# Optimization experiments

Measured on AMD Instinct MI355X. Metric: run time of the kernel, lower is better.

Reference implementation:

```python
import jax, jax.numpy as jnp
import numpy as np

B, S, H, R = 2, 1024, 512, 64


def setup_inputs() -> dict:
    key = jax.random.key(0)
    k1, k2, k3 = jax.random.split(key, 3)
    hidden_states = jax.random.normal(k1, (B, S, H), dtype=jnp.float32)
    # all_indices is the row-major cartesian product (seq_idx, hidden_idx),
    # as required by the final .view(batch, seq_len, hidden_size) in the module.
    si = jnp.repeat(jnp.arange(S, dtype=jnp.int64), H)
    hi = jnp.tile(jnp.arange(H, dtype=jnp.int64), S)
    all_indices = jnp.stack([si, hi], axis=1)  # [S*H, 2]
    W_seq = jax.random.normal(k2, (R, H), dtype=jnp.float32) * (1.0 / np.sqrt(H))
    hidden_embeddings = jax.random.normal(k3, (H, R), dtype=jnp.float32) * 0.02
    cp_weight = jnp.ones((1, R), dtype=jnp.float32)  # CP buffer, all ones
    return {
        "hidden_states": hidden_states,
        "all_indices": all_indices,
        "W_seq": W_seq,
        "hidden_embeddings": hidden_embeddings,
        "cp_weight": cp_weight,
    }


def reference(hidden_states, all_indices, W_seq, hidden_embeddings, cp_weight):
    b, s, h = hidden_states.shape
    # seq_mode_factor: Linear(hidden_size -> rank), no bias
    seq_emb = jnp.einsum("bsh,rh->bsr", hidden_states, W_seq)  # [B,S,R]
    si = all_indices[:, 0]  # [N]
    hi = all_indices[:, 1]  # [N]
    # Fold the (all-ones) CP weight into the hidden-mode factor, then
    # gather + hadamard + rank reduction in one fused expression.
    hid_fac = hidden_embeddings * cp_weight[0][None, :]  # [H,R]
    out = jnp.einsum("bnr,nr->bn", seq_emb[:, si, :], hid_fac[hi, :])  # [B,N]
    n = all_indices.shape[0]
    return out.reshape(b, s, n // s)  # [B,S,H], out_units=1 squeezed
```

## Files before the change

kernel.cpp:

```cpp
#include <hip/hip_runtime.h>


#define Hd 512
#define Rd 64
#define ROWS 8
#define THREADS 256

__global__ __launch_bounds__(THREADS) void cp_fused(
    const float* __restrict__ hs,
    const float* __restrict__ W,
    const float* __restrict__ he,
    const float* __restrict__ cp,
    float* __restrict__ out)
{
    __shared__ float s_hs[ROWS][Hd];
    __shared__ float s_E[ROWS][Rd];
    __shared__ float s_cp[Rd];

    const int t = threadIdx.x;
    const size_t row0 = (size_t)blockIdx.x * ROWS;

    const float4* hs4 = (const float4*)(hs + row0 * Hd);
    float4* s_hs4 = (float4*)&s_hs[0][0];
#pragma unroll
    for (int i = 0; i < 4; ++i)
        s_hs4[t + i * THREADS] = hs4[t + i * THREADS];
    if (t < Rd) s_cp[t] = cp[t];
    __syncthreads();

    {
        const int r = t >> 2;
        const int q = t & 3;
        float acc[ROWS];
#pragma unroll
        for (int i = 0; i < ROWS; ++i) acc[i] = 0.f;
        const float4* w4 = (const float4*)(W + r * Hd + q * 128);
#pragma unroll 8
        for (int j = 0; j < 32; ++j) {
            const float4 w = w4[j];
#pragma unroll
            for (int i = 0; i < ROWS; ++i) {
                const float4 x = ((const float4*)&s_hs[i][q * 128])[j];
                acc[i] += w.x * x.x + w.y * x.y + w.z * x.z + w.w * x.w;
            }
        }
#pragma unroll
        for (int i = 0; i < ROWS; ++i) {
            acc[i] += __shfl_xor(acc[i], 1);
            acc[i] += __shfl_xor(acc[i], 2);
        }
        if (q == 0) {
#pragma unroll
            for (int i = 0; i < ROWS; ++i) s_E[i][r] = acc[i];
        }
    }
    __syncthreads();

#pragma unroll
    for (int hh = 0; hh < 2; ++hh) {
        const int h = t + hh * THREADS;
        float o[ROWS];
#pragma unroll
        for (int i = 0; i < ROWS; ++i) o[i] = 0.f;
        const float4* he4 = (const float4*)(he + h * Rd);
#pragma unroll
        for (int j = 0; j < 16; ++j) {
            float4 f = he4[j];
            f.x *= s_cp[4 * j + 0];
            f.y *= s_cp[4 * j + 1];
            f.z *= s_cp[4 * j + 2];
            f.w *= s_cp[4 * j + 3];
#pragma unroll
            for (int i = 0; i < ROWS; ++i) {
                o[i] += s_E[i][4 * j + 0] * f.x + s_E[i][4 * j + 1] * f.y
                      + s_E[i][4 * j + 2] * f.z + s_E[i][4 * j + 3] * f.w;
            }
        }
#pragma unroll
        for (int i = 0; i < ROWS; ++i)
            out[(row0 + i) * Hd + h] = o[i];
    }
}

extern "C" void kernel_launch(void* const* d_in, const int* in_sizes, int n_in,
                              void* d_out, int out_size, void* d_ws, size_t ws_size,
                              hipStream_t stream) {
    const float* hs = (const float*)d_in[0];
    const float* W  = (const float*)d_in[2];
    const float* he = (const float*)d_in[3];
    const float* cp = (const float*)d_in[4];
    float* out = (float*)d_out;

    const int n_rows = 2 * 1024;
    cp_fused<<<dim3(n_rows / ROWS), dim3(THREADS), 0, stream>>>(hs, W, he, cp, out);
}
```

Baseline: 87.88 us.

## Stage W and hidden embeddings through padded shared memory with register prefetch

Both matmul phases now stream their weight matrices (W_seq, then hidden_embeddings) through a padded shared-memory buffer in four chunks. The next chunk is prefetched into registers while the current one is computed. Work is remapped so each thread reads one padded weight row from LDS against a broadcast activation row: two sequence rows per wave in phase one, four output rows per thread in phase two. This removes the strided per-thread global loads and the cross-lane shuffle reduction, at the cost of extra syncs and about 34KB more shared memory, which could reduce occupancy.

```diff
diff --git a/kernel.cpp b/kernel.cpp
--- a/kernel.cpp
+++ b/kernel.cpp
@@ -4,9 +4,11 @@
 #define Hd 512
 #define Rd 64
 #define ROWS 8
-#define THREADS 256
+#define T 256
+#define WPAD 132
+#define HPAD 68
 
-__global__ __launch_bounds__(THREADS) void cp_fused(
+__global__ __launch_bounds__(T) void cp_fused_v2(
     const float* __restrict__ hs,
     const float* __restrict__ W,
     const float* __restrict__ he,
@@ -14,71 +16,99 @@
     float* __restrict__ out)
 {
     __shared__ float s_hs[ROWS][Hd];
+    __shared__ float s_buf[128 * HPAD];
     __shared__ float s_E[ROWS][Rd];
     __shared__ float s_cp[Rd];
 
     const int t = threadIdx.x;
+    const int lane = t & 63;
+    const int w = t >> 6;
     const size_t row0 = (size_t)blockIdx.x * ROWS;
 
     const float4* hs4 = (const float4*)(hs + row0 * Hd);
     float4* s_hs4 = (float4*)&s_hs[0][0];
 #pragma unroll
-    for (int i = 0; i < 4; ++i)
-        s_hs4[t + i * THREADS] = hs4[t + i * THREADS];
+    for (int i = 0; i < 4; ++i) s_hs4[t + i * T] = hs4[t + i * T];
     if (t < Rd) s_cp[t] = cp[t];
-    __syncthreads();
 
-    {
-        const int r = t >> 2;
-        const int q = t & 3;
-        float acc[ROWS];
+    const int rw = t >> 5;
+    const int q4 = t & 31;
+
+    float4 pfw[8];
 #pragma unroll
-        for (int i = 0; i < ROWS; ++i) acc[i] = 0.f;
-        const float4* w4 = (const float4*)(W + r * Hd + q * 128);
-#pragma unroll 8
+    for (int k = 0; k < 8; ++k)
+        pfw[k] = ((const float4*)W)[(rw + 8 * k) * 128 + q4];
+
+    const int r0 = 2 * w, r1 = 2 * w + 1;
+    float acc0 = 0.f, acc1 = 0.f;
+
+    for (int c = 0; c < 4; ++c) {
+        __syncthreads();
+#pragma unroll
+        for (int k = 0; k < 8; ++k)
+            *(float4*)&s_buf[(rw + 8 * k) * WPAD + 4 * q4] = pfw[k];
+        __syncthreads();
+        if (c < 3) {
+#pragma unroll
+            for (int k = 0; k < 8; ++k)
+                pfw[k] = ((const float4*)W)[(rw + 8 * k) * 128 + (c + 1) * 32 + q4];
+        }
+        const float* wrow = &s_buf[lane * WPAD];
+        const float* h0p = &s_hs[r0][c * 128];
+        const float* h1p = &s_hs[r1][c * 128];
+#pragma unroll
         for (int j = 0; j < 32; ++j) {
-            const float4 w = w4[j];
-#pragma unroll
-            for (int i = 0; i < ROWS; ++i) {
-                const float4 x = ((const float4*)&s_hs[i][q * 128])[j];
-                acc[i] += w.x * x.x + w.y * x.y + w.z * x.z + w.w * x.w;
-            }
-        }
-#pragma unroll
-        for (int i = 0; i < ROWS; ++i) {
-            acc[i] += __shfl_xor(acc[i], 1);
-            acc[i] += __shfl_xor(acc[i], 2);
-        }
-        if (q == 0) {
-#pragma unroll
-            for (int i = 0; i < ROWS; ++i) s_E[i][r] = acc[i];
+            const float4 wt = *(const float4*)&wrow[4 * j];
+            const float4 a  = *(const float4*)&h0p[4 * j];
+            const float4 b  = *(const float4*)&h1p[4 * j];
+            acc0 += wt.x * a.x + wt.y * a.y + wt.z * a.z + wt.w * a.w;
+            acc1 += wt.x * b.x + wt.y * b.y + wt.z * b.z + wt.w * b.w;
         }
     }
-    __syncthreads();
+    const float cpl = s_cp[lane];
+    s_E[r0][lane] = acc0 * cpl;
+    s_E[r1][lane] = acc1 * cpl;
 
+    float4 pfh[8];
 #pragma unroll
-    for (int hh = 0; hh < 2; ++hh) {
-        const int h = t + hh * THREADS;
-        float o[ROWS];
+    for (int k = 0; k < 8; ++k)
+        pfh[k] = ((const float4*)he)[t + k * T];
+
+    const int hl = t & 127;
+    const int rb = (t >> 7) * 4;
+
+    for (int c = 0; c < 4; ++c) {
+        __syncthreads();
 #pragma unroll
-        for (int i = 0; i < ROWS; ++i) o[i] = 0.f;
-        const float4* he4 = (const float4*)(he + h * Rd);
+        for (int k = 0; k < 8; ++k) {
+            const int f = t + k * T;
+            *(float4*)&s_buf[(f >> 4) * HPAD + 4 * (f & 15)] = pfh[k];
+        }
+        __syncthreads();
+        if (c < 3) {
+#pragma unroll
+            for (int k = 0; k < 8; ++k)
+                pfh[k] = ((const float4*)he)[(c + 1) * 2048 + t + k * T];
+        }
+        float o0 = 0.f, o1 = 0.f, o2 = 0.f, o3 = 0.f;
+        const float* hrow = &s_buf[hl * HPAD];
 #pragma unroll
         for (int j = 0; j < 16; ++j) {
-            float4 f = he4[j];
-            f.x *= s_cp[4 * j + 0];
-            f.y *= s_cp[4 * j + 1];
-            f.z *= s_cp[4 * j + 2];
-            f.w *= s_cp[4 * j + 3];
-#pragma unroll
-            for (int i = 0; i < ROWS; ++i) {
-                o[i] += s_E[i][4 * j + 0] * f.x + s_E[i][4 * j + 1] * f.y
-                      + s_E[i][4 * j + 2] * f.z + s_E[i][4 * j + 3] * f.w;
-            }
+            const float4 hf = *(const float4*)&hrow[4 * j];
+            const float4 e0 = *(const float4*)&s_E[rb + 0][4 * j];
+            const float4 e1 = *(const float4*)&s_E[rb + 1][4 * j];
+            const float4 e2 = *(const float4*)&s_E[rb + 2][4 * j];
+            const float4 e3 = *(const float4*)&s_E[rb + 3][4 * j];
+            o0 += hf.x * e0.x + hf.y * e0.y + hf.z * e0.z + hf.w * e0.w;
+            o1 += hf.x * e1.x + hf.y * e1.y + hf.z * e1.z + hf.w * e1.w;
+            o2 += hf.x * e2.x + hf.y * e2.y + hf.z * e2.z + hf.w * e2.w;
+            o3 += hf.x * e3.x + hf.y * e3.y + hf.z * e3.z + hf.w * e3.w;
         }
-#pragma unroll
-        for (int i = 0; i < ROWS; ++i)
-            out[(row0 + i) * Hd + h] = o[i];
+        float* op = out + (row0 + rb) * Hd + c * 128 + hl;
+        op[0 * Hd] = o0;
+        op[1 * Hd] = o1;
+        op[2 * Hd] = o2;
+        op[3 * Hd] = o3;
     }
 }
 
@@ -91,6 +121,5 @@
     const float* cp = (const float*)d_in[4];
     float* out = (float*)d_out;
 
-    const int n_rows = 2 * 1024;
-    cp_fused<<<dim3(n_rows / ROWS), dim3(THREADS), 0, stream>>>(hs, W, he, cp, out);
+    cp_fused_v2<<<dim3(2048 / ROWS), dim3(T), 0, stream>>>(hs, W, he, cp, out);
 }
```

After: 92.75 us. +5.6%, slower.

## Precompute combined hidden-to-hidden matrix and replace low-rank path with single GEMM

Applied to the files above, without the earlier changes.

Splits the work into two kernels: one that folds W_seq, the CP weight and the hidden embeddings into a dense HxH matrix K in workspace, and a GEMM kernel that multiplies hidden_states by K with a split-K reduction through shared memory. This removes the two-stage rank-64 contraction and its intermediate synchronization. In exchange it raises arithmetic per row about fourfold, adds a second launch and writes and reads a 1 MB intermediate.

```diff
diff --git a/kernel.cpp b/kernel.cpp
--- a/kernel.cpp
+++ b/kernel.cpp
@@ -3,82 +3,114 @@
 
 #define Hd 512
 #define Rd 64
-#define ROWS 8
-#define THREADS 256
 
-__global__ __launch_bounds__(THREADS) void cp_fused(
-    const float* __restrict__ hs,
+__global__ __launch_bounds__(256) void cp_precompute_K(
     const float* __restrict__ W,
     const float* __restrict__ he,
     const float* __restrict__ cp,
+    float* __restrict__ K)
+{
+    __shared__ float s_W[8][Rd];
+    __shared__ float s_he[128 * 65];
+
+    const int t = threadIdx.x;
+    const int hp0 = blockIdx.x * 8;
+
+    {
+        const int i = t & 7, r = t >> 3;
+        s_W[i][r]      = W[r * Hd + hp0 + i] * cp[r];
+        s_W[i][r + 32] = W[(r + 32) * Hd + hp0 + i] * cp[r + 32];
+    }
+
+    const int hl = t & 127;
+    const int ig = (t >> 7) * 4;
+
+    for (int hc = 0; hc < 4; ++hc) {
+        __syncthreads();
+        const float4* src = (const float4*)(he + (size_t)hc * 128 * Rd);
+#pragma unroll
+        for (int k = 0; k < 8; ++k) {
+            const int f = t + k * 256;
+            const int h = f >> 4, r4 = f & 15;
+            const float4 v = src[f];
+            float* d = &s_he[h * 65 + 4 * r4];
+            d[0] = v.x; d[1] = v.y; d[2] = v.z; d[3] = v.w;
+        }
+        __syncthreads();
+
+        float a0 = 0.f, a1 = 0.f, a2 = 0.f, a3 = 0.f;
+        const float* hrow = &s_he[hl * 65];
+#pragma unroll
+        for (int r = 0; r < Rd; ++r) {
+            const float hv = hrow[r];
+            a0 += hv * s_W[ig + 0][r];
+            a1 += hv * s_W[ig + 1][r];
+            a2 += hv * s_W[ig + 2][r];
+            a3 += hv * s_W[ig + 3][r];
+        }
+        const int h = hc * 128 + hl;
+        K[(hp0 + ig + 0) * Hd + h] = a0;
+        K[(hp0 + ig + 1) * Hd + h] = a1;
+        K[(hp0 + ig + 2) * Hd + h] = a2;
+        K[(hp0 + ig + 3) * Hd + h] = a3;
+    }
+}
+
+__global__ __launch_bounds__(512) void cp_gemm(
+    const float* __restrict__ hs,
+    const float* __restrict__ K,
     float* __restrict__ out)
 {
-    __shared__ float s_hs[ROWS][Hd];
-    __shared__ float s_E[ROWS][Rd];
-    __shared__ float s_cp[Rd];
+    __shared__ float s_hs[8][Hd];
+    __shared__ float2 s_red[256][9];
 
     const int t = threadIdx.x;
-    const size_t row0 = (size_t)blockIdx.x * ROWS;
-
-    const float4* hs4 = (const float4*)(hs + row0 * Hd);
-    float4* s_hs4 = (float4*)&s_hs[0][0];
-#pragma unroll
-    for (int i = 0; i < 4; ++i)
-        s_hs4[t + i * THREADS] = hs4[t + i * THREADS];
-    if (t < Rd) s_cp[t] = cp[t];
-    __syncthreads();
+    const size_t row0 = (size_t)blockIdx.x * 8;
 
     {
-        const int r = t >> 2;
-        const int q = t & 3;
-        float acc[ROWS];
-#pragma unroll
-        for (int i = 0; i < ROWS; ++i) acc[i] = 0.f;
-        const float4* w4 = (const float4*)(W + r * Hd + q * 128);
-#pragma unroll 8
-        for (int j = 0; j < 32; ++j) {
-            const float4 w = w4[j];
-#pragma unroll
-            for (int i = 0; i < ROWS; ++i) {
-                const float4 x = ((const float4*)&s_hs[i][q * 128])[j];
-                acc[i] += w.x * x.x + w.y * x.y + w.z * x.z + w.w * x.w;
-            }
-        }
-#pragma unroll
-        for (int i = 0; i < ROWS; ++i) {
-            acc[i] += __shfl_xor(acc[i], 1);
-            acc[i] += __shfl_xor(acc[i], 2);
-        }
-        if (q == 0) {
-#pragma unroll
-            for (int i = 0; i < ROWS; ++i) s_E[i][r] = acc[i];
-        }
+        const float4* src = (const float4*)(hs + row0 * Hd);
+        float4* dst = (float4*)&s_hs[0][0];
+        dst[t] = src[t];
+        dst[t + 512] = src[t + 512];
     }
     __syncthreads();
 
+    const int hcol = t & 255;
+    const int half = t >> 8;
+    const int hpB = half * 256;
+
+    float2 acc[8];
 #pragma unroll
-    for (int hh = 0; hh < 2; ++hh) {
-        const int h = t + hh * THREADS;
-        float o[ROWS];
+    for (int i = 0; i < 8; ++i) acc[i] = make_float2(0.f, 0.f);
+
+    const float2* K2 = (const float2*)K;
+
+    for (int hp = 0; hp < 256; hp += 4) {
+        float2 kv0 = K2[(hpB + hp + 0) * 256 + hcol];
+        float2 kv1 = K2[(hpB + hp + 1) * 256 + hcol];
+        float2 kv2 = K2[(hpB + hp + 2) * 256 + hcol];
+        float2 kv3 = K2[(hpB + hp + 3) * 256 + hcol];
 #pragma unroll
-        for (int i = 0; i < ROWS; ++i) o[i] = 0.f;
-        const float4* he4 = (const float4*)(he + h * Rd);
+        for (int i = 0; i < 8; ++i) {
+            const float4 a = *(const float4*)&s_hs[i][hpB + hp];
+            acc[i].x += a.x * kv0.x + a.y * kv1.x + a.z * kv2.x + a.w * kv3.x;
+            acc[i].y += a.x * kv0.y + a.y * kv1.y + a.z * kv2.y + a.w * kv3.y;
+        }
+    }
+
+    if (half == 1) {
 #pragma unroll
-        for (int j = 0; j < 16; ++j) {
-            float4 f = he4[j];
-            f.x *= s_cp[4 * j + 0];
-            f.y *= s_cp[4 * j + 1];
-            f.z *= s_cp[4 * j + 2];
-            f.w *= s_cp[4 * j + 3];
+        for (int i = 0; i < 8; ++i) s_red[hcol][i] = acc[i];
+    }
+    __syncthreads();
+    if (half == 0) {
 #pragma unroll
-            for (int i = 0; i < ROWS; ++i) {
-                o[i] += s_E[i][4 * j + 0] * f.x + s_E[i][4 * j + 1] * f.y
-                      + s_E[i][4 * j + 2] * f.z + s_E[i][4 * j + 3] * f.w;
-            }
+        for (int i = 0; i < 8; ++i) {
+            const float2 p = s_red[hcol][i];
+            acc[i].x += p.x;
+            acc[i].y += p.y;
+            *(float2*)&out[(row0 + i) * Hd + 2 * hcol] = acc[i];
         }
-#pragma unroll
-        for (int i = 0; i < ROWS; ++i)
-            out[(row0 + i) * Hd + h] = o[i];
     }
 }
 
@@ -90,7 +122,8 @@
     const float* he = (const float*)d_in[3];
     const float* cp = (const float*)d_in[4];
     float* out = (float*)d_out;
+    float* Kbuf = (float*)d_ws;
 
-    const int n_rows = 2 * 1024;
-    cp_fused<<<dim3(n_rows / ROWS), dim3(THREADS), 0, stream>>>(hs, W, he, cp, out);
+    cp_precompute_K<<<dim3(64), dim3(256), 0, stream>>>(W, he, cp, Kbuf);
+    cp_gemm<<<dim3(256), dim3(512), 0, stream>>>(hs, Kbuf, out);
 }
```

Measured after the change: 115.5 us. 1.31x slower.

## Precompute combined weight matrix and run single bf16 MFMA GEMM

Applied to the files above, without the earlier changes.

Reassociates the two chained projections by first building K = (he*cp)·W as a 512x512 bf16 matrix in a small kernel, then computing out = hs·K^T with a bf16 MFMA GEMM. This removes the rank-64 intermediate and the per-block reload of W and he in favour of tensor-core matrix ops with a swizzled tile order. It adds a second launch and workspace traffic, raises FLOPs (512x512 inner product instead of two rank-64 passes), and lowers precision by rounding both hs and K to bf16.

```diff
diff --git a/kernel.cpp b/kernel.cpp
--- a/kernel.cpp
+++ b/kernel.cpp
@@ -1,85 +1,78 @@
 #include <hip/hip_runtime.h>
 
 
-#define Hd 512
-#define Rd 64
-#define ROWS 8
-#define THREADS 256
+typedef __bf16 bf16x8 __attribute__((ext_vector_type(8)));
+typedef float f32x4 __attribute__((ext_vector_type(4)));
 
-__global__ __launch_bounds__(THREADS) void cp_fused(
-    const float* __restrict__ hs,
+__global__ __launch_bounds__(256) void cp_K(
     const float* __restrict__ W,
     const float* __restrict__ he,
     const float* __restrict__ cp,
-    float* __restrict__ out)
+    __bf16* __restrict__ KT)
 {
-    __shared__ float s_hs[ROWS][Hd];
-    __shared__ float s_E[ROWS][Rd];
-    __shared__ float s_cp[Rd];
-
+    __shared__ float s_he[2][64];
     const int t = threadIdx.x;
-    const size_t row0 = (size_t)blockIdx.x * ROWS;
-
-    const float4* hs4 = (const float4*)(hs + row0 * Hd);
-    float4* s_hs4 = (float4*)&s_hs[0][0];
-#pragma unroll
-    for (int i = 0; i < 4; ++i)
-        s_hs4[t + i * THREADS] = hs4[t + i * THREADS];
-    if (t < Rd) s_cp[t] = cp[t];
-    __syncthreads();
-
-    {
-        const int r = t >> 2;
-        const int q = t & 3;
-        float acc[ROWS];
-#pragma unroll
-        for (int i = 0; i < ROWS; ++i) acc[i] = 0.f;
-        const float4* w4 = (const float4*)(W + r * Hd + q * 128);
-#pragma unroll 8
-        for (int j = 0; j < 32; ++j) {
-            const float4 w = w4[j];
-#pragma unroll
-            for (int i = 0; i < ROWS; ++i) {
-                const float4 x = ((const float4*)&s_hs[i][q * 128])[j];
-                acc[i] += w.x * x.x + w.y * x.y + w.z * x.z + w.w * x.w;
-            }
-        }
-#pragma unroll
-        for (int i = 0; i < ROWS; ++i) {
-            acc[i] += __shfl_xor(acc[i], 1);
-            acc[i] += __shfl_xor(acc[i], 2);
-        }
-        if (q == 0) {
-#pragma unroll
-            for (int i = 0; i < ROWS; ++i) s_E[i][r] = acc[i];
-        }
+    const int h0 = blockIdx.x * 2;
+    if (t < 128) {
+        const int hh = t >> 6, r = t & 63;
+        s_he[hh][r] = he[(h0 + hh) * 64 + r] * cp[r];
     }
     __syncthreads();
 
-#pragma unroll
-    for (int hh = 0; hh < 2; ++hh) {
-        const int h = t + hh * THREADS;
-        float o[ROWS];
-#pragma unroll
-        for (int i = 0; i < ROWS; ++i) o[i] = 0.f;
-        const float4* he4 = (const float4*)(he + h * Rd);
-#pragma unroll
-        for (int j = 0; j < 16; ++j) {
-            float4 f = he4[j];
-            f.x *= s_cp[4 * j + 0];
-            f.y *= s_cp[4 * j + 1];
-            f.z *= s_cp[4 * j + 2];
-            f.w *= s_cp[4 * j + 3];
-#pragma unroll
-            for (int i = 0; i < ROWS; ++i) {
-                o[i] += s_E[i][4 * j + 0] * f.x + s_E[i][4 * j + 1] * f.y
-                      + s_E[i][4 * j + 2] * f.z + s_E[i][4 * j + 3] * f.w;
-            }
-        }
-#pragma unroll
-        for (int i = 0; i < ROWS; ++i)
-            out[(row0 + i) * Hd + h] = o[i];
+    float a00 = 0.f, a01 = 0.f, a10 = 0.f, a11 = 0.f;
+#pragma unroll 8
+    for (int r = 0; r < 64; ++r) {
+        const float w0 = W[r * 512 + t];
+        const float w1 = W[r * 512 + t + 256];
+        const float e0 = s_he[0][r];
+        const float e1 = s_he[1][r];
+        a00 += e0 * w0; a01 += e0 * w1;
+        a10 += e1 * w0; a11 += e1 * w1;
     }
+    KT[(size_t)h0 * 512 + t]             = (__bf16)a00;
+    KT[(size_t)h0 * 512 + t + 256]       = (__bf16)a01;
+    KT[(size_t)(h0 + 1) * 512 + t]       = (__bf16)a10;
+    KT[(size_t)(h0 + 1) * 512 + t + 256] = (__bf16)a11;
+}
+
+__global__ __launch_bounds__(256) void cp_gemm_mfma(
+    const float* __restrict__ hs,
+    const __bf16* __restrict__ KT,
+    float* __restrict__ out)
+{
+    const int t = threadIdx.x;
+    const int w = t >> 6;
+    const int L = t & 63;
+    const int mq = L & 15;
+    const int kq = L >> 4;
+
+    const int bx = blockIdx.x;
+    const int idx = (bx & 7) * 128 + (bx >> 3);
+    const int mt = idx >> 4, nt = idx & 15;
+
+    const int m0 = mt * 32 + (w >> 1) * 16;
+    const int n0 = nt * 32 + (w & 1) * 16;
+
+    const float*  aRow = hs + (size_t)(m0 + mq) * 512 + kq * 8;
+    const __bf16* bRow = KT + (size_t)(n0 + mq) * 512 + kq * 8;
+
+    f32x4 acc = {0.f, 0.f, 0.f, 0.f};
+#pragma unroll 4
+    for (int ks = 0; ks < 16; ++ks) {
+        const float4 f0 = *(const float4*)(aRow + ks * 32);
+        const float4 f1 = *(const float4*)(aRow + ks * 32 + 4);
+        const bf16x8 b  = *(const bf16x8*)(bRow + ks * 32);
+        bf16x8 a;
+        a[0] = (__bf16)f0.x; a[1] = (__bf16)f0.y; a[2] = (__bf16)f0.z; a[3] = (__bf16)f0.w;
+        a[4] = (__bf16)f1.x; a[5] = (__bf16)f1.y; a[6] = (__bf16)f1.z; a[7] = (__bf16)f1.w;
+        acc = __builtin_amdgcn_mfma_f32_16x16x32_bf16(a, b, acc, 0, 0, 0);
+    }
+
+    float* op = out + (size_t)(m0 + kq * 4) * 512 + n0 + mq;
+    op[0]        = acc[0];
+    op[512]      = acc[1];
+    op[2 * 512]  = acc[2];
+    op[3 * 512]  = acc[3];
 }
 
 extern "C" void kernel_launch(void* const* d_in, const int* in_sizes, int n_in,
@@ -90,7 +83,8 @@
     const float* he = (const float*)d_in[3];
     const float* cp = (const float*)d_in[4];
     float* out = (float*)d_out;
+    __bf16* KT = (__bf16*)d_ws;
 
-    const int n_rows = 2 * 1024;
-    cp_fused<<<dim3(n_rows / ROWS), dim3(THREADS), 0, stream>>>(hs, W, he, cp, out);
+    cp_K<<<dim3(256), dim3(256), 0, stream>>>(W, he, cp, KT);
+    cp_gemm_mfma<<<dim3(1024), dim3(256), 0, stream>>>(hs, KT, out);
 }
```

After: 89.58 us. Within noise of the previous version (+1.9%).
